# Kernel tuning notes

Hardware: AMD Instinct MI355X
Metric: run time of the kernel (lower is better)

Reference implementation:

```python
import jax, jax.numpy as jnp
import numpy as np

# so(3) generators (3x3x3), L[s, r, a]
L = jnp.array([[[0, 0, 0], [0, 0, -1], [0, 1, 0]],
               [[0, 0, 1], [0, 0, 0], [-1, 0, 0]],
               [[0, -1, 0], [1, 0, 0], [0, 0, 0]]], dtype=jnp.float32)


def setup_inputs() -> dict:
    key = jax.random.key(0)
    B, S, X, Y = 32, 3, 512, 512
    s = jax.random.normal(key, (B, S, X, Y), dtype=jnp.float32)
    # normalize to unit O(3) spins (physically realistic; math identical for any s)
    s = s / jnp.linalg.norm(s, axis=1, keepdims=True)
    t = jnp.ones((1,), dtype=jnp.float32)   # flow time
    c0 = jnp.ones((1,), dtype=jnp.float32)  # learnable coefficient C[0]
    return {"s": s, "t": t, "c0": c0}


def reference(s, t, c0):
    # Psi11t.grad(s, t): flow force of the (psi_1^1)^2 action term.
    # Coeff(t) with EvenOdd=False and cc=[c0] is t * c0.
    coeff = t * c0  # shape [1], broadcasts

    def nbr(x, mu):
        # sum of forward and backward periodic neighbors along lattice axis mu
        return jnp.roll(x, -1, axis=mu) + jnp.roll(x, 1, axis=mu)

    # b[b,x,y] = sum_mu s . (s shifted +/- along mu)
    b = (jnp.einsum('bsxy,bsxy->bxy', s, nbr(s, 2))
         + jnp.einsum('bsxy,bsxy->bxy', s, nbr(s, 3)))

    bs = s * b[:, None]  # [B,3,X,Y]

    # Lsig[b,r,a,x,y] = -sum_s s[b,s,x,y] * L[s,r,a]
    Lsig = -jnp.einsum('bsxy,sra->braxy', s, L)

    Fs = nbr(s, 2) + nbr(s, 3)      # [B,3,X,Y]
    Fbs = nbr(bs, 2) + nbr(bs, 3)   # [B,3,X,Y]

    F = Fs * b[:, None] + Fbs
    F = jnp.einsum('bsaxy,bsxy->baxy', Lsig, F)  # so(3) generator contraction
    return 2.0 * coeff * F
```

## Files before the change

kernel.cpp:

```cpp
#include <hip/hip_runtime.h>

#define BATCH 32
#define NX 512
#define NY 512
#define XY (NX * NY)

typedef float floatx4 __attribute__((ext_vector_type(4)));

__global__ __launch_bounds__(256) void psi11t_kernel(
    const float* __restrict__ s,
    const float* __restrict__ t,
    const float* __restrict__ c0,
    float* __restrict__ out)
{
    const int D = blockIdx.x;
    const int L = (D & 7) * 1024 + (D >> 3);
    const int bidx  = L >> 8;
    const int strip = L & 255;

    const int tid = threadIdx.x;
    const int yg  = tid & 127;
    const int xr  = tid >> 7;
    const int y0  = yg * 4;
    const int x   = strip * 2 + xr;

    const int xm1 = (x + NX - 1) & (NX - 1);
    const int xp1 = (x + 1)      & (NX - 1);
    const int xm2 = (x + NX - 2) & (NX - 1);
    const int xp2 = (x + 2)      & (NX - 1);
    const int om4 = (y0 + NY - 4) & (NY - 1);
    const int op4 = (y0 + 4)      & (NY - 1);

    const float* sb = s + (size_t)bidx * 3 * XY;

    float cm[3][12], um[3][12], dm[3][12], u2[3][4], d2[3][4];

    #pragma unroll
    for (int c = 0; c < 3; ++c) {
        const float* base = sb + (size_t)c * XY;
        const float* rc  = base + (size_t)x   * NY;
        const float* rm  = base + (size_t)xm1 * NY;
        const float* rp  = base + (size_t)xp1 * NY;
        const float* rm2 = base + (size_t)xm2 * NY;
        const float* rp2 = base + (size_t)xp2 * NY;

        *(floatx4*)&cm[c][0] = *(const floatx4*)(rc + om4);
        *(floatx4*)&cm[c][4] = *(const floatx4*)(rc + y0);
        *(floatx4*)&cm[c][8] = *(const floatx4*)(rc + op4);
        *(floatx4*)&um[c][0] = *(const floatx4*)(rm + om4);
        *(floatx4*)&um[c][4] = *(const floatx4*)(rm + y0);
        *(floatx4*)&um[c][8] = *(const floatx4*)(rm + op4);
        *(floatx4*)&dm[c][0] = *(const floatx4*)(rp + om4);
        *(floatx4*)&dm[c][4] = *(const floatx4*)(rp + y0);
        *(floatx4*)&dm[c][8] = *(const floatx4*)(rp + op4);
        *(floatx4*)&u2[c][0] = *(const floatx4*)(rm2 + y0);
        *(floatx4*)&d2[c][0] = *(const floatx4*)(rp2 + y0);
    }

    const float coeff = 2.0f * t[0] * c0[0];

    float o[3][4];
    #pragma unroll
    for (int i = 0; i < 4; ++i) {
        float sc[3], sA[3], sB[3], sC[3], sD[3], Fs[3];
        float bc = 0.f, bA = 0.f, bB = 0.f, bC = 0.f, bD = 0.f;
        #pragma unroll
        for (int c = 0; c < 3; ++c) {
            sc[c] = cm[c][4 + i];
            sC[c] = cm[c][3 + i];
            sD[c] = cm[c][5 + i];
            float sCC = cm[c][2 + i];
            float sDD = cm[c][6 + i];
            sA[c] = um[c][4 + i];
            float sAC = um[c][3 + i];
            float sAD = um[c][5 + i];
            sB[c] = dm[c][4 + i];
            float sBC = dm[c][3 + i];
            float sBD = dm[c][5 + i];
            float sAA = u2[c][i];
            float sBB = d2[c][i];

            float nsum = sA[c] + sB[c] + sC[c] + sD[c];
            Fs[c] = nsum;
            bc += sc[c] * nsum;
            bA += sA[c] * (sAA + sc[c] + sAC + sAD);
            bB += sB[c] * (sc[c] + sBB + sBC + sBD);
            bC += sC[c] * (sAC + sBC + sCC + sc[c]);
            bD += sD[c] * (sAD + sBD + sc[c] + sDD);
        }
        float G[3];
        #pragma unroll
        for (int c = 0; c < 3; ++c)
            G[c] = Fs[c] * bc + sA[c] * bA + sB[c] * bB + sC[c] * bC + sD[c] * bD;
        o[0][i] = (sc[1] * G[2] - sc[2] * G[1]) * coeff;
        o[1][i] = (sc[2] * G[0] - sc[0] * G[2]) * coeff;
        o[2][i] = (sc[0] * G[1] - sc[1] * G[0]) * coeff;
    }

    float* ob = out + (size_t)bidx * 3 * XY + (size_t)x * NY + y0;
    floatx4 v0 = { o[0][0], o[0][1], o[0][2], o[0][3] };
    floatx4 v1 = { o[1][0], o[1][1], o[1][2], o[1][3] };
    floatx4 v2 = { o[2][0], o[2][1], o[2][2], o[2][3] };
    __builtin_nontemporal_store(v0, (floatx4*)(ob));
    __builtin_nontemporal_store(v1, (floatx4*)(ob + XY));
    __builtin_nontemporal_store(v2, (floatx4*)(ob + 2 * XY));
}

extern "C" void kernel_launch(void* const* d_in, const int* in_sizes, int n_in,
                              void* d_out, int out_size, void* d_ws, size_t ws_size,
                              hipStream_t stream) {
    const float* s  = (const float*)d_in[0];
    const float* t  = (const float*)d_in[1];
    const float* c0 = (const float*)d_in[2];
    float* out = (float*)d_out;

    psi11t_kernel<<<8192, 256, 0, stream>>>(s, t, c0, out);
}
```

Measured before the change: 209.0 us.

## Compute two adjacent rows per thread and share the b-field between them

Each thread now produces output for two consecutive x rows instead of one. It loads a 6-row stencil window and computes the neighbour dot-product field b once for the shared rows, so the b values and the loads are reused across both outputs. The grid is halved to 4096 blocks. This cuts redundant global loads and recomputation of b per output element, but raises register pressure and lowers occupancy and parallelism.

```diff
diff --git a/kernel.cpp b/kernel.cpp
--- a/kernel.cpp
+++ b/kernel.cpp
@@ -14,96 +14,116 @@
     float* __restrict__ out)
 {
     const int D = blockIdx.x;
-    const int L = (D & 7) * 1024 + (D >> 3);
-    const int bidx  = L >> 8;
-    const int strip = L & 255;
+    const int L = (D & 7) * 512 + (D >> 3);
+    const int bidx  = L >> 7;
+    const int strip = L & 127;
 
     const int tid = threadIdx.x;
     const int yg  = tid & 127;
     const int xr  = tid >> 7;
     const int y0  = yg * 4;
-    const int x   = strip * 2 + xr;
+    const int x   = strip * 4 + xr * 2;
 
+    const int xm2 = (x + NX - 2) & (NX - 1);
     const int xm1 = (x + NX - 1) & (NX - 1);
-    const int xp1 = (x + 1)      & (NX - 1);
-    const int xm2 = (x + NX - 2) & (NX - 1);
-    const int xp2 = (x + 2)      & (NX - 1);
+    const int xp1 = x + 1;
+    const int xp2 = (x + 2) & (NX - 1);
+    const int xp3 = (x + 3) & (NX - 1);
     const int om4 = (y0 + NY - 4) & (NY - 1);
     const int op4 = (y0 + 4)      & (NY - 1);
 
     const float* sb = s + (size_t)bidx * 3 * XY;
 
-    float cm[3][12], um[3][12], dm[3][12], u2[3][4], d2[3][4];
+    float A2m[3][4], Am[3][12], C0[3][12], C1[3][12], Bp[3][12], B2p[3][4];
 
     #pragma unroll
     for (int c = 0; c < 3; ++c) {
         const float* base = sb + (size_t)c * XY;
-        const float* rc  = base + (size_t)x   * NY;
-        const float* rm  = base + (size_t)xm1 * NY;
-        const float* rp  = base + (size_t)xp1 * NY;
         const float* rm2 = base + (size_t)xm2 * NY;
+        const float* rm1 = base + (size_t)xm1 * NY;
+        const float* r0  = base + (size_t)x   * NY;
+        const float* r1  = base + (size_t)xp1 * NY;
         const float* rp2 = base + (size_t)xp2 * NY;
+        const float* rp3 = base + (size_t)xp3 * NY;
 
-        *(floatx4*)&cm[c][0] = *(const floatx4*)(rc + om4);
-        *(floatx4*)&cm[c][4] = *(const floatx4*)(rc + y0);
-        *(floatx4*)&cm[c][8] = *(const floatx4*)(rc + op4);
-        *(floatx4*)&um[c][0] = *(const floatx4*)(rm + om4);
-        *(floatx4*)&um[c][4] = *(const floatx4*)(rm + y0);
-        *(floatx4*)&um[c][8] = *(const floatx4*)(rm + op4);
-        *(floatx4*)&dm[c][0] = *(const floatx4*)(rp + om4);
-        *(floatx4*)&dm[c][4] = *(const floatx4*)(rp + y0);
-        *(floatx4*)&dm[c][8] = *(const floatx4*)(rp + op4);
-        *(floatx4*)&u2[c][0] = *(const floatx4*)(rm2 + y0);
-        *(floatx4*)&d2[c][0] = *(const floatx4*)(rp2 + y0);
+        *(floatx4*)&A2m[c][0] = *(const floatx4*)(rm2 + y0);
+        *(floatx4*)&Am[c][0]  = *(const floatx4*)(rm1 + om4);
+        *(floatx4*)&Am[c][4]  = *(const floatx4*)(rm1 + y0);
+        *(floatx4*)&Am[c][8]  = *(const floatx4*)(rm1 + op4);
+        *(floatx4*)&C0[c][0]  = *(const floatx4*)(r0 + om4);
+        *(floatx4*)&C0[c][4]  = *(const floatx4*)(r0 + y0);
+        *(floatx4*)&C0[c][8]  = *(const floatx4*)(r0 + op4);
+        *(floatx4*)&C1[c][0]  = *(const floatx4*)(r1 + om4);
+        *(floatx4*)&C1[c][4]  = *(const floatx4*)(r1 + y0);
+        *(floatx4*)&C1[c][8]  = *(const floatx4*)(r1 + op4);
+        *(floatx4*)&Bp[c][0]  = *(const floatx4*)(rp2 + om4);
+        *(floatx4*)&Bp[c][4]  = *(const floatx4*)(rp2 + y0);
+        *(floatx4*)&Bp[c][8]  = *(const floatx4*)(rp2 + op4);
+        *(floatx4*)&B2p[c][0] = *(const floatx4*)(rp3 + y0);
     }
 
     const float coeff = 2.0f * t[0] * c0[0];
 
-    float o[3][4];
+    float b0[6], b1[6], bm[4], bp2[4];
+
+    #pragma unroll
+    for (int j = 0; j < 6; ++j) {
+        float a0 = 0.f, a1 = 0.f;
+        #pragma unroll
+        for (int c = 0; c < 3; ++c) {
+            a0 += C0[c][3 + j] * (Am[c][3 + j] + C1[c][3 + j] + C0[c][2 + j] + C0[c][4 + j]);
+            a1 += C1[c][3 + j] * (C0[c][3 + j] + Bp[c][3 + j] + C1[c][2 + j] + C1[c][4 + j]);
+        }
+        b0[j] = a0;
+        b1[j] = a1;
+    }
     #pragma unroll
     for (int i = 0; i < 4; ++i) {
-        float sc[3], sA[3], sB[3], sC[3], sD[3], Fs[3];
-        float bc = 0.f, bA = 0.f, bB = 0.f, bC = 0.f, bD = 0.f;
+        float am = 0.f, ap = 0.f;
         #pragma unroll
         for (int c = 0; c < 3; ++c) {
-            sc[c] = cm[c][4 + i];
-            sC[c] = cm[c][3 + i];
-            sD[c] = cm[c][5 + i];
-            float sCC = cm[c][2 + i];
-            float sDD = cm[c][6 + i];
-            sA[c] = um[c][4 + i];
-            float sAC = um[c][3 + i];
-            float sAD = um[c][5 + i];
-            sB[c] = dm[c][4 + i];
-            float sBC = dm[c][3 + i];
-            float sBD = dm[c][5 + i];
-            float sAA = u2[c][i];
-            float sBB = d2[c][i];
+            am += Am[c][4 + i] * (A2m[c][i] + C0[c][4 + i] + Am[c][3 + i] + Am[c][5 + i]);
+            ap += Bp[c][4 + i] * (C1[c][4 + i] + B2p[c][i] + Bp[c][3 + i] + Bp[c][5 + i]);
+        }
+        bm[i]  = am;
+        bp2[i] = ap;
+    }
 
-            float nsum = sA[c] + sB[c] + sC[c] + sD[c];
-            Fs[c] = nsum;
-            bc += sc[c] * nsum;
-            bA += sA[c] * (sAA + sc[c] + sAC + sAD);
-            bB += sB[c] * (sc[c] + sBB + sBC + sBD);
-            bC += sC[c] * (sAC + sBC + sCC + sc[c]);
-            bD += sD[c] * (sAD + sBD + sc[c] + sDD);
+    float o0[3][4], o1[3][4];
+    #pragma unroll
+    for (int i = 0; i < 4; ++i) {
+        float G0[3], G1[3];
+        #pragma unroll
+        for (int c = 0; c < 3; ++c) {
+            float Fs0 = Am[c][4 + i] + C1[c][4 + i] + C0[c][3 + i] + C0[c][5 + i];
+            G0[c] = Fs0 * b0[1 + i]
+                  + Am[c][4 + i] * bm[i]
+                  + C1[c][4 + i] * b1[1 + i]
+                  + C0[c][3 + i] * b0[i]
+                  + C0[c][5 + i] * b0[2 + i];
+            float Fs1 = C0[c][4 + i] + Bp[c][4 + i] + C1[c][3 + i] + C1[c][5 + i];
+            G1[c] = Fs1 * b1[1 + i]
+                  + C0[c][4 + i] * b0[1 + i]
+                  + Bp[c][4 + i] * bp2[i]
+                  + C1[c][3 + i] * b1[i]
+                  + C1[c][5 + i] * b1[2 + i];
         }
-        float G[3];
-        #pragma unroll
-        for (int c = 0; c < 3; ++c)
-            G[c] = Fs[c] * bc + sA[c] * bA + sB[c] * bB + sC[c] * bC + sD[c] * bD;
-        o[0][i] = (sc[1] * G[2] - sc[2] * G[1]) * coeff;
-        o[1][i] = (sc[2] * G[0] - sc[0] * G[2]) * coeff;
-        o[2][i] = (sc[0] * G[1] - sc[1] * G[0]) * coeff;
+        o0[0][i] = (C0[1][4 + i] * G0[2] - C0[2][4 + i] * G0[1]) * coeff;
+        o0[1][i] = (C0[2][4 + i] * G0[0] - C0[0][4 + i] * G0[2]) * coeff;
+        o0[2][i] = (C0[0][4 + i] * G0[1] - C0[1][4 + i] * G0[0]) * coeff;
+        o1[0][i] = (C1[1][4 + i] * G1[2] - C1[2][4 + i] * G1[1]) * coeff;
+        o1[1][i] = (C1[2][4 + i] * G1[0] - C1[0][4 + i] * G1[2]) * coeff;
+        o1[2][i] = (C1[0][4 + i] * G1[1] - C1[1][4 + i] * G1[0]) * coeff;
     }
 
     float* ob = out + (size_t)bidx * 3 * XY + (size_t)x * NY + y0;
-    floatx4 v0 = { o[0][0], o[0][1], o[0][2], o[0][3] };
-    floatx4 v1 = { o[1][0], o[1][1], o[1][2], o[1][3] };
-    floatx4 v2 = { o[2][0], o[2][1], o[2][2], o[2][3] };
-    __builtin_nontemporal_store(v0, (floatx4*)(ob));
-    __builtin_nontemporal_store(v1, (floatx4*)(ob + XY));
-    __builtin_nontemporal_store(v2, (floatx4*)(ob + 2 * XY));
+    #pragma unroll
+    for (int c = 0; c < 3; ++c) {
+        floatx4 v0 = { o0[c][0], o0[c][1], o0[c][2], o0[c][3] };
+        floatx4 v1 = { o1[c][0], o1[c][1], o1[c][2], o1[c][3] };
+        __builtin_nontemporal_store(v0, (floatx4*)(ob + (size_t)c * XY));
+        __builtin_nontemporal_store(v1, (floatx4*)(ob + (size_t)c * XY + NY));
+    }
 }
 
 extern "C" void kernel_launch(void* const* d_in, const int* in_sizes, int n_in,
@@ -114,5 +134,5 @@
     const float* c0 = (const float*)d_in[2];
     float* out = (float*)d_out;
 
-    psi11t_kernel<<<8192, 256, 0, stream>>>(s, t, c0, out);
+    psi11t_kernel<<<4096, 256, 0, stream>>>(s, t, c0, out);
 }
```

Result: faster. 193.8 us (-7.3%).
